# Optimization experiments

Hardware: AMD Instinct MI355X
Metric: run time of the kernel (lower is better)

The kernel has to match this reference:

```python
import jax, jax.numpy as jnp
import numpy as np

BLOCK = 4  # block_size from init_kwargs


def space_to_channel_3d(x, b):
    # Faithful translation of SpaceToChannel_3d.forward (torch split/stack/permute chain).
    B, C, W, H, D = x.shape
    y = x.transpose(0, 2, 3, 4, 1)                      # (B, W, H, D, C)
    y = y.reshape(B, W, H, D // b, b, C)                # split depth into D//b chunks of b
    y = y.transpose(0, 3, 1, 2, 4, 5)                   # (B, D//b, W, H, b, C)
    y = y.reshape(B, D // b, W // b, H // b, C * b * b * b)  # per-chunk row-major reshape
    y = y.transpose(0, 2, 3, 1, 4)                      # (B, W//b, H//b, D//b, C*b^3)
    return y.transpose(0, 4, 1, 2, 3)                   # (B, C*b^3, W//b, H//b, D//b)


def channel_to_space_3d(x, b):
    # Faithful translation of ChannelToSpace_3d.forward.
    B, Cd, wd, hd, dd = x.shape
    b3 = b * b * b
    Cs = Cd // b3
    y = x.transpose(0, 2, 3, 4, 1)                      # (B, wd, hd, dd, Cd)
    y = y.reshape(B, wd, hd, dd, b * b, b, Cs)          # split b^3 dim into b^2 chunks of b
    y = y.transpose(0, 4, 1, 2, 3, 5, 6)                # (B, b^2, wd, hd, dd, b, Cs)
    y = y.reshape(B, b * b, wd, hd, dd * b, Cs)         # merge (dd, b) per chunk
    y = y.transpose(0, 2, 1, 3, 4, 5)                   # (B, wd, b^2, hd, dd*b, Cs)
    y = y.reshape(B, wd * b, hd * b, dd * b, Cs)        # row-major merge of (wd, b^2, hd)
    return y.transpose(0, 4, 1, 2, 3)                   # (B, Cs, wd*b, hd*b, dd*b)


def setup_inputs() -> dict:
    key = jax.random.key(0)
    k1, k2 = jax.random.split(key)
    x = jax.random.normal(k1, (4, 32, 64, 64, 64), dtype=jnp.float32)
    gamma = jax.random.normal(k2, (1,), dtype=jnp.float32)
    return {"x": x, "gamma": gamma}


def reference(x, gamma):
    b = BLOCK
    y = space_to_channel_3d(x, b)                       # (B, C*b^3, w, h, d)
    B, C, w, h, d = y.shape
    q = y.reshape(B, C, w * h * d)                      # (B, C', N)
    # channel-wise attention: energy (B, C', C')
    energy = jnp.einsum('bcn,ben->bce', q, q)
    energy_new = jnp.max(energy, axis=-1, keepdims=True) - energy
    attention = jax.nn.softmax(energy_new, axis=-1)
    out = jnp.einsum('bce,ben->bcn', attention, q)      # (B, C', N)
    out = out.reshape(B, C, w, h, d)
    out = gamma * out + y
    return channel_to_space_3d(out, b)
```

## Files before the change

### kernel.cpp

```cpp
#include <hip/hip_runtime.h>

typedef _Float16 f16;
typedef __attribute__((ext_vector_type(8))) _Float16 f16x8;
typedef __attribute__((ext_vector_type(4))) float f32x4;

#define CCH 2048
#define NSP 4096
#define NB  4

__device__ __forceinline__ void gld16(const void* g, void* l) {
  __builtin_amdgcn_global_load_lds(
      (const __attribute__((address_space(1))) void*)g,
      (__attribute__((address_space(3))) void*)l, 16, 0, 0);
}

__global__ void pack_kernel(const float* __restrict__ x, f16* __restrict__ qh,
                            f16* __restrict__ ql, int b0) {
  int gid = blockIdx.x * 256 + threadIdx.x;
  int n = gid & (NSP - 1);
  int t = gid >> 12;
  int c = t & 31; t >>= 5;
  int r = t & 15; int ib = t >> 4;
  int wc = n >> 8, hc = (n >> 4) & 15, dc = n & 15;
  int w = wc * 4 + (hc >> 2);
  int h = (hc & 3) * 16 + r;
  int b = b0 + ib;
  const f32x4 v = *(const f32x4*)(x + ((((size_t)b * 32 + c) * 64 + w) * 64 + h) * 64 + dc * 4);
#pragma unroll
  for (int bd = 0; bd < 4; ++bd) {
    int cc = r * 128 + bd * 32 + c;
    size_t o = ((size_t)ib * CCH + cc) * NSP + n;
    float val = v[bd];
    f16 hi = (f16)val;
    qh[o] = hi;
    ql[o] = (f16)(val - (float)hi);
  }
}

__global__ void transpose_kernel(const f16* __restrict__ qh, f16* __restrict__ qhT) {
  int ib = blockIdx.z;
  int j0 = blockIdx.x * 64, n0 = blockIdx.y * 64;
  __shared__ f16 tile[64][72];
  int t = threadIdx.x;
  int r = t >> 3;
  int cb = (t & 7) * 8;
#pragma unroll
  for (int half = 0; half < 2; ++half) {
    int rr = r + half * 32;
    f16x8 v = *(const f16x8*)(qh + ((size_t)ib * CCH + j0 + rr) * NSP + n0 + cb);
    *(f16x8*)&tile[rr][cb] = v;
  }
  __syncthreads();
#pragma unroll
  for (int half = 0; half < 2; ++half) {
    int rr = r + half * 32;
    f16x8 o;
#pragma unroll
    for (int u = 0; u < 8; ++u) o[u] = tile[cb + u][rr];
    *(f16x8*)(qhT + ((size_t)ib * NSP + n0 + rr) * CCH + j0 + cb) = o;
  }
}

__global__ __launch_bounds__(256) void gemm1_kernel(const f16* __restrict__ qh,
                                                    const f16* __restrict__ ql,
                                                    float* __restrict__ energy) {
  int ib = blockIdx.z;
  int bx = blockIdx.x;
  int tri = (bx & 7) * 17 + (bx >> 3);
  int rem = tri, bi = 0, span = 16;
  while (rem >= span) { rem -= span; ++bi; --span; }
  int bj = bi + rem;
  int i0 = bi * 128, j0 = bj * 128;
  float* eout = energy + (size_t)ib * CCH * CCH;

  __shared__ f16 Lds[2][4][128 * 32];
  int tid = threadIdx.x;
  int lane = tid & 63, wv = tid >> 6;
  int l15 = lane & 15, quad = lane >> 4;
  int wr = (wv >> 1) * 64, wcol = (wv & 1) * 64;
  int swz = (l15 >> 1) & 3;
  int kbs = (lane & 3) ^ ((lane >> 3) & 3);

  const f16* srcA = (wv & 1) ? ql : qh;
  int rbase = (wv < 2) ? i0 : j0;
  const f16* gsrc = srcA + ((size_t)ib * CCH + rbase) * NSP
                    + (size_t)(lane >> 2) * NSP + kbs * 8;

  auto stage = [&](int buf, int kk) {
    f16* ld = &Lds[buf][wv][0];
#pragma unroll
    for (int t = 0; t < 8; ++t)
      gld16(gsrc + (size_t)(t * 16) * NSP + kk, ld + t * 512);
  };

  const f32x4 vzero = {0.f, 0.f, 0.f, 0.f};
  f32x4 acc[4][4];
#pragma unroll
  for (int a = 0; a < 4; ++a)
#pragma unroll
    for (int bq = 0; bq < 4; ++bq) acc[a][bq] = vzero;

  const int nk = NSP >> 5;
  stage(0, 0);
  __syncthreads();
  for (int it = 0; it < nk; ++it) {
    int cur = it & 1;
    if (it + 1 < nk) stage(cur ^ 1, (it + 1) << 5);
    f16x8 ah[4], al[4], bh[4], bl[4];
#pragma unroll
    for (int mt = 0; mt < 4; ++mt) {
      int row = wr + mt * 16 + l15;
      ah[mt] = *(const f16x8*)&Lds[cur][0][row * 32 + ((quad ^ swz) * 8)];
      al[mt] = *(const f16x8*)&Lds[cur][1][row * 32 + ((quad ^ swz) * 8)];
    }
#pragma unroll
    for (int nt = 0; nt < 4; ++nt) {
      int col = wcol + nt * 16 + l15;
      bh[nt] = *(const f16x8*)&Lds[cur][2][col * 32 + ((quad ^ swz) * 8)];
      bl[nt] = *(const f16x8*)&Lds[cur][3][col * 32 + ((quad ^ swz) * 8)];
    }
    __builtin_amdgcn_s_setprio(1);
#pragma unroll
    for (int mt = 0; mt < 4; ++mt)
#pragma unroll
      for (int nt = 0; nt < 4; ++nt) {
        acc[mt][nt] = __builtin_amdgcn_mfma_f32_16x16x32_f16(ah[mt], bh[nt], acc[mt][nt], 0, 0, 0);
        acc[mt][nt] = __builtin_amdgcn_mfma_f32_16x16x32_f16(ah[mt], bl[nt], acc[mt][nt], 0, 0, 0);
        acc[mt][nt] = __builtin_amdgcn_mfma_f32_16x16x32_f16(al[mt], bh[nt], acc[mt][nt], 0, 0, 0);
      }
    __builtin_amdgcn_s_setprio(0);
    __syncthreads();
  }
  bool diag = (bi == bj);
#pragma unroll
  for (int mt = 0; mt < 4; ++mt)
#pragma unroll
    for (int nt = 0; nt < 4; ++nt)
#pragma unroll
      for (int rg = 0; rg < 4; ++rg) {
        int row = i0 + wr + mt * 16 + quad * 4 + rg;
        int col = j0 + wcol + nt * 16 + l15;
        float v = acc[mt][nt][rg];
        eout[(size_t)row * CCH + col] = v;
        if (!diag) eout[(size_t)col * CCH + row] = v;
      }
}

__global__ void softmax_kernel(const float* __restrict__ e0,
                               const float* __restrict__ gamma_p,
                               f16* __restrict__ attn) {
  int i = blockIdx.x, ib = blockIdx.y;
  const float* r0 = e0 + ((size_t)ib * CCH + i) * CCH;
  f16* arow = attn + ((size_t)ib * CCH + i) * CCH;
  int t = threadIdx.x;
  f32x4 v0 = *(const f32x4*)(r0 + t * 8);
  f32x4 v1 = *(const f32x4*)(r0 + t * 8 + 4);
  float m = v0[0];
#pragma unroll
  for (int u = 1; u < 4; ++u) m = fminf(m, v0[u]);
#pragma unroll
  for (int u = 0; u < 4; ++u) m = fminf(m, v1[u]);
#pragma unroll
  for (int off = 32; off > 0; off >>= 1) m = fminf(m, __shfl_xor(m, off));
  __shared__ float redA[4], redB[4];
  if ((t & 63) == 0) redA[t >> 6] = m;
  __syncthreads();
  m = fminf(fminf(redA[0], redA[1]), fminf(redA[2], redA[3]));
  float e[8], s = 0.f;
#pragma unroll
  for (int u = 0; u < 4; ++u) { e[u] = __expf(m - v0[u]); s += e[u]; }
#pragma unroll
  for (int u = 0; u < 4; ++u) { e[4 + u] = __expf(m - v1[u]); s += e[4 + u]; }
#pragma unroll
  for (int off = 32; off > 0; off >>= 1) s += __shfl_xor(s, off);
  if ((t & 63) == 0) redB[t >> 6] = s;
  __syncthreads();
  s = redB[0] + redB[1] + redB[2] + redB[3];
  float gamma = *gamma_p;
  float ginv = gamma / s;
  int du = i - t * 8;
  f16x8 o;
#pragma unroll
  for (int u = 0; u < 8; ++u) {
    float v = e[u] * ginv;
    if (u == du) v += 1.0f;
    o[u] = (f16)v;
  }
  *(f16x8*)(arow + t * 8) = o;
}

__global__ __launch_bounds__(512) void gemm2_kernel(const f16* __restrict__ attn,
                                                    const f16* __restrict__ qhT,
                                                    float* __restrict__ out, int b0) {
  int ib = blockIdx.z;
  int lin = blockIdx.x + gridDim.x * blockIdx.y;
  int nwg = gridDim.x * gridDim.y;
  int cpx = nwg >> 3;
  int lin2 = (lin & 7) * cpx + (lin >> 3);
  int i0 = (lin2 & 7) * 256;
  int n0 = (lin2 >> 3) * 256;
  __shared__ f16 Lds[2][2][256 * 32];
  int tid = threadIdx.x;
  int lane = tid & 63, wv = tid >> 6;
  int l15 = lane & 15, quad = lane >> 4;
  int wr = (wv >> 2) * 128;
  int wcol = (wv & 3) * 64;
  int swz = (l15 >> 1) & 3;
  int kbs = (lane & 3) ^ ((lane >> 3) & 3);

  int arr = wv >> 2, rsub = wv & 3;
  const f16* gbase = arr ? (qhT + ((size_t)ib * NSP + n0) * CCH)
                         : (attn + ((size_t)ib * CCH + i0) * CCH);
  const f16* gsrc = gbase + (size_t)(rsub * 64 + (lane >> 2)) * CCH + kbs * 8;

  auto stage = [&](int buf, int kk) {
#pragma unroll
    for (int t = 0; t < 4; ++t)
      gld16(gsrc + (size_t)(t * 16) * CCH + kk,
            &Lds[buf][arr][(rsub * 64 + t * 16) * 32]);
  };

  const f32x4 vzero = {0.f, 0.f, 0.f, 0.f};
  f32x4 acc[8][4];
#pragma unroll
  for (int a = 0; a < 8; ++a)
#pragma unroll
    for (int bq = 0; bq < 4; ++bq) acc[a][bq] = vzero;

  const int nk = CCH >> 5;
  stage(0, 0);
  __syncthreads();
  for (int it = 0; it < nk; ++it) {
    int cur = it & 1;
    if (it + 1 < nk) stage(cur ^ 1, (it + 1) << 5);
    f16x8 af[8], bf[4];
#pragma unroll
    for (int mt = 0; mt < 8; ++mt)
      af[mt] = *(const f16x8*)&Lds[cur][0][(wr + mt * 16 + l15) * 32 + ((quad ^ swz) * 8)];
#pragma unroll
    for (int nt = 0; nt < 4; ++nt)
      bf[nt] = *(const f16x8*)&Lds[cur][1][(wcol + nt * 16 + l15) * 32 + ((quad ^ swz) * 8)];
    __builtin_amdgcn_s_setprio(1);
#pragma unroll
    for (int mt = 0; mt < 8; ++mt)
#pragma unroll
      for (int nt = 0; nt < 4; ++nt)
        acc[mt][nt] = __builtin_amdgcn_mfma_f32_16x16x32_f16(af[mt], bf[nt], acc[mt][nt], 0, 0, 0);
    __builtin_amdgcn_s_setprio(0);
    __syncthreads();
  }

  float* eld = (float*)&Lds[0][0][0];
  int b = b0 + ib;
#pragma unroll
  for (int p = 0; p < 4; ++p) {
    __syncthreads();
    if ((wv >> 1) == p) {
#pragma unroll
      for (int mt = 0; mt < 8; ++mt) {
        int f = mt >> 1;
        int gb2 = (mt & 1) * 16 + quad * 4;
#pragma unroll
        for (int nt = 0; nt < 4; ++nt) {
          int jh = (wv & 1) * 4 + nt;
#pragma unroll
          for (int rg = 0; rg < 4; ++rg)
            eld[(gb2 + rg) * 512 + jh * 64 + l15 * 4 + f] = acc[mt][nt][rg];
        }
      }
    }
    __syncthreads();
    int h = p >> 1, nh = p & 1;
    int e = (i0 >> 7) + h;
    int W = (n0 >> 8) * 4 + (e >> 2);
    int H0 = (e & 3) * 16 + nh * 8;
#pragma unroll
    for (int u = 0; u < 4; ++u) {
      int g = wv * 4 + u;
      size_t goff = ((((size_t)b * 32 + g) * 64 + W) * 4096) + (size_t)H0 * 64;
#pragma unroll
      for (int hv = 0; hv < 2; ++hv) {
        int fo = hv * 256 + lane * 4;
        *(f32x4*)(out + goff + fo) = *(const f32x4*)&eld[g * 512 + fo];
      }
    }
  }
}

extern "C" void kernel_launch(void* const* d_in, const int* in_sizes, int n_in,
                              void* d_out, int out_size, void* d_ws, size_t ws_size,
                              hipStream_t stream) {
  const float* x = (const float*)d_in[0];
  const float* gamma = (const float*)d_in[1];
  float* out = (float*)d_out;

  const size_t szQ = (size_t)CCH * NSP;
  const size_t szE = (size_t)CCH * CCH;

  const size_t pb = szQ * 2 * 3 + szE * 4 + szE * 2;

  int nb = (ws_size >= (size_t)NB * pb) ? NB : 1;

  char* p = (char*)d_ws;
  f16* qh = (f16*)p;   p += (size_t)nb * szQ * 2;
  f16* ql = (f16*)p;   p += (size_t)nb * szQ * 2;
  f16* qhT = (f16*)p;  p += (size_t)nb * szQ * 2;
  float* energy = (float*)p; p += (size_t)nb * szE * 4;
  f16* attn = (f16*)p;

  for (int b0 = 0; b0 < NB; b0 += nb) {
    pack_kernel<<<nb * 8192, 256, 0, stream>>>(x, qh, ql, b0);
    transpose_kernel<<<dim3(32, 64, nb), 256, 0, stream>>>(qh, qhT);
    gemm1_kernel<<<dim3(136, 1, nb), 256, 0, stream>>>(qh, ql, energy);
    softmax_kernel<<<dim3(CCH, nb), 256, 0, stream>>>(energy, gamma, attn);
    gemm2_kernel<<<dim3(8, 16, nb), 512, 0, stream>>>(attn, qhT, out, b0);
  }
}
```

Measured before the change: 749.0 us.

## Split gemm1 K dimension in two and sum partial energies in softmax

Adds a split-K mode to the energy GEMM that doubles the workgroup count (136 to 272 per batch) with each half covering 2048 of the 4096 spatial elements and writing its own partial energy buffer. The softmax kernel then reads both partials and adds them before the row reduction. The aim is better CU occupancy on the 256-CU device, where 544 workgroups across 4 batches leave many CUs idle. The cost is a second energy buffer of extra workspace plus doubled energy write and read traffic.

Measured after the change: 689.2 us. -8.0%, faster.

```diff
diff --git a/kernel.cpp b/kernel.cpp
--- a/kernel.cpp
+++ b/kernel.cpp
@@ -63,15 +63,22 @@
 
 __global__ __launch_bounds__(256) void gemm1_kernel(const f16* __restrict__ qh,
                                                     const f16* __restrict__ ql,
-                                                    float* __restrict__ energy) {
+                                                    float* __restrict__ energy,
+                                                    int ksplit) {
   int ib = blockIdx.z;
+  int nwg = gridDim.x;
+  int cpx = nwg >> 3;
   int bx = blockIdx.x;
-  int tri = (bx & 7) * 17 + (bx >> 3);
+  int tri = (bx & 7) * cpx + (bx >> 3);
+  int ks = 0;
+  if (ksplit == 2) { ks = tri >= 136; tri -= ks * 136; }
   int rem = tri, bi = 0, span = 16;
   while (rem >= span) { rem -= span; ++bi; --span; }
   int bj = bi + rem;
   int i0 = bi * 128, j0 = bj * 128;
-  float* eout = energy + (size_t)ib * CCH * CCH;
+  int kbeg = ks * 2048;
+  int kend = (ksplit == 2) ? kbeg + 2048 : NSP;
+  float* eout = energy + ((size_t)(ks * gridDim.z + ib)) * CCH * CCH;
 
   __shared__ f16 Lds[2][4][128 * 32];
   int tid = threadIdx.x;
@@ -100,12 +107,12 @@
 #pragma unroll
     for (int bq = 0; bq < 4; ++bq) acc[a][bq] = vzero;
 
-  const int nk = NSP >> 5;
-  stage(0, 0);
+  int nk = (kend - kbeg) >> 5;
+  stage(0, kbeg);
   __syncthreads();
   for (int it = 0; it < nk; ++it) {
     int cur = it & 1;
-    if (it + 1 < nk) stage(cur ^ 1, (it + 1) << 5);
+    if (it + 1 < nk) stage(cur ^ 1, kbeg + ((it + 1) << 5));
     f16x8 ah[4], al[4], bh[4], bl[4];
 #pragma unroll
     for (int mt = 0; mt < 4; ++mt) {
@@ -146,15 +153,22 @@
       }
 }
 
-__global__ void softmax_kernel(const float* __restrict__ e0,
-                               const float* __restrict__ gamma_p,
+__global__ void softmax_kernel(const float* __restrict__ e0, const float* __restrict__ e1,
+                               int two, const float* __restrict__ gamma_p,
                                f16* __restrict__ attn) {
   int i = blockIdx.x, ib = blockIdx.y;
   const float* r0 = e0 + ((size_t)ib * CCH + i) * CCH;
+  const float* r1 = e1 + ((size_t)ib * CCH + i) * CCH;
   f16* arow = attn + ((size_t)ib * CCH + i) * CCH;
   int t = threadIdx.x;
   f32x4 v0 = *(const f32x4*)(r0 + t * 8);
   f32x4 v1 = *(const f32x4*)(r0 + t * 8 + 4);
+  if (two) {
+    f32x4 u0 = *(const f32x4*)(r1 + t * 8);
+    f32x4 u1 = *(const f32x4*)(r1 + t * 8 + 4);
+#pragma unroll
+    for (int u = 0; u < 4; ++u) { v0[u] += u0[u]; v1[u] += u1[u]; }
+  }
   float m = v0[0];
 #pragma unroll
   for (int u = 1; u < 4; ++u) m = fminf(m, v0[u]);
@@ -297,22 +311,27 @@
   const size_t szQ = (size_t)CCH * NSP;
   const size_t szE = (size_t)CCH * CCH;
 
-  const size_t pb = szQ * 2 * 3 + szE * 4 + szE * 2;
-
-  int nb = (ws_size >= (size_t)NB * pb) ? NB : 1;
+  const size_t pbSplit = szQ * 2 * 3 + szE * 4 * 2 + szE * 2;
+  const size_t pbNoSplit = szQ * 2 * 3 + szE * 4 + szE * 2;
+
+  int ksplit, nb;
+  if (ws_size >= (size_t)NB * pbSplit) { ksplit = 2; nb = NB; }
+  else if (ws_size >= (size_t)NB * pbNoSplit) { ksplit = 1; nb = NB; }
+  else { ksplit = 1; nb = 1; }
 
   char* p = (char*)d_ws;
   f16* qh = (f16*)p;   p += (size_t)nb * szQ * 2;
   f16* ql = (f16*)p;   p += (size_t)nb * szQ * 2;
   f16* qhT = (f16*)p;  p += (size_t)nb * szQ * 2;
-  float* energy = (float*)p; p += (size_t)nb * szE * 4;
+  float* energy = (float*)p; p += (size_t)nb * szE * 4 * ksplit;
   f16* attn = (f16*)p;
+  const float* e1 = (ksplit == 2) ? (energy + (size_t)nb * szE) : energy;
 
   for (int b0 = 0; b0 < NB; b0 += nb) {
     pack_kernel<<<nb * 8192, 256, 0, stream>>>(x, qh, ql, b0);
     transpose_kernel<<<dim3(32, 64, nb), 256, 0, stream>>>(qh, qhT);
-    gemm1_kernel<<<dim3(136, 1, nb), 256, 0, stream>>>(qh, ql, energy);
-    softmax_kernel<<<dim3(CCH, nb), 256, 0, stream>>>(energy, gamma, attn);
+    gemm1_kernel<<<dim3(136 * ksplit, 1, nb), 256, 0, stream>>>(qh, ql, energy, ksplit);
+    softmax_kernel<<<dim3(CCH, nb), 256, 0, stream>>>(energy, e1, ksplit - 1, gamma, attn);
     gemm2_kernel<<<dim3(8, 16, nb), 512, 0, stream>>>(attn, qhT, out, b0);
   }
 }
```
